# Optimization experiments

Hardware: AMD Instinct MI355X
Metric: run time of the kernel (lower is better)

## Reference

```python
import jax, jax.numpy as jnp
import numpy as np

B, S, D_MODEL, H = 2, 2048, 1024, 16
HD = D_MODEL // H  # head_dim = 64


def setup_inputs() -> dict:
    key = jax.random.key(0)
    kx, kq, kk, kv, ko = jax.random.split(key, 5)
    scale = 1.0 / np.sqrt(D_MODEL)
    return {
        "x": jax.random.normal(kx, (B, S, D_MODEL), dtype=jnp.float32),
        "Wq": jax.random.normal(kq, (D_MODEL, D_MODEL), dtype=jnp.float32) * scale,
        "Wk": jax.random.normal(kk, (D_MODEL, D_MODEL), dtype=jnp.float32) * scale,
        "Wv": jax.random.normal(kv, (D_MODEL, D_MODEL), dtype=jnp.float32) * scale,
        "Wo": jax.random.normal(ko, (D_MODEL, D_MODEL), dtype=jnp.float32) * scale,
        "bo": jnp.zeros((D_MODEL,), dtype=jnp.float32),
    }


def reference(x, Wq, Wk, Wv, Wo, bo):
    b, s, _ = x.shape
    # project and split heads: [b, h, s, hd]
    q = (x @ Wq).reshape(b, s, H, HD).transpose(0, 2, 1, 3)
    k = (x @ Wk).reshape(b, s, H, HD).transpose(0, 2, 1, 3)
    v = (x @ Wv).reshape(b, s, H, HD).transpose(0, 2, 1, 3)
    # full attn score materialization, as in the original module
    scores = jnp.einsum("bhqd,bhkd->bhqk", q, k)
    causal = jnp.triu(jnp.ones((s, s), dtype=bool), k=1)  # True above diagonal -> masked
    scores = jnp.where(causal, -jnp.inf, scores)
    attn = jax.nn.softmax(scores / np.sqrt(HD), axis=-1)  # dropout p=0.0 (eval)
    ctx = jnp.einsum("bhqk,bhkd->bqhd", attn, v).reshape(b, s, D_MODEL)
    return ctx @ Wo + bo
```

## Files before the change

### kernel.cpp

```cpp
#include <hip/hip_runtime.h>
#include <stdint.h>

typedef __bf16 bf16x8 __attribute__((ext_vector_type(8)));
typedef float f32x4 __attribute__((ext_vector_type(4)));

static constexpr int B_ = 2, S_ = 2048, D_ = 1024, H_ = 16, HD_ = 64;
static constexpr int M_ = B_ * S_;
static constexpr size_t HSZ = (size_t)B_ * H_ * S_ * HD_;

#define DEV_INLINE __device__ __forceinline__

#define SC2F (0.125f * 1.4426950408889634f)

DEV_INLINE uint16_t f2bf(float f) {
  __bf16 h = (__bf16)f;
  return __builtin_bit_cast(uint16_t, h);
}

#define GLD16(gptr, lptr)                                                        \
  __builtin_amdgcn_global_load_lds(                                              \
      (const __attribute__((address_space(1))) void*)(gptr),                     \
      (__attribute__((address_space(3))) void*)(lptr), 16, 0, 0)

__global__ void cvt_x_kernel(const float* __restrict__ x, uint16_t* __restrict__ xb) {
  int i = blockIdx.x * 256 + threadIdx.x;
  float4 v = reinterpret_cast<const float4*>(x)[i];
  ushort4 o;
  o.x = f2bf(v.x); o.y = f2bf(v.y); o.z = f2bf(v.z); o.w = f2bf(v.w);
  reinterpret_cast<ushort4*>(xb)[i] = o;
}

__global__ void tr_w_kernel(const float* __restrict__ W0, const float* __restrict__ W1,
                            const float* __restrict__ W2, const float* __restrict__ W3,
                            uint16_t* __restrict__ Wt) {
  __shared__ float tile[32][33];
  const float* W = (blockIdx.z == 0) ? W0 : (blockIdx.z == 1) ? W1
                   : (blockIdx.z == 2) ? W2 : W3;
  uint16_t* dst = Wt + (size_t)blockIdx.z * D_ * D_;
  int c = blockIdx.x * 32 + threadIdx.x;
  int r0 = blockIdx.y * 32;
#pragma unroll
  for (int j = threadIdx.y; j < 32; j += 8)
    tile[j][threadIdx.x] = W[(size_t)(r0 + j) * D_ + c];
  __syncthreads();
  int oc = blockIdx.y * 32 + threadIdx.x;
  int or0 = blockIdx.x * 32;
#pragma unroll
  for (int j = threadIdx.y; j < 32; j += 8)
    dst[(size_t)(or0 + j) * D_ + oc] = f2bf(tile[threadIdx.x][j]);
}

template <int EPI>
__global__ __launch_bounds__(256, 2)
void gemm_bt_kernel(const uint16_t* __restrict__ A, const uint16_t* __restrict__ Bt,
                    uint16_t* __restrict__ Cb, float* __restrict__ Cf,
                    const float* __restrict__ bias, int K) {
  __shared__ uint16_t lds[2][2][128 * 32];
  const int tid = threadIdx.x;
  const int lane = tid & 63;
  const int wid = tid >> 6;
  const int lo = lane & 15, hi = lane >> 4;
  const int row0 = blockIdx.y * 128, col0 = blockIdx.x * 128;
  const int wr = (wid >> 1) * 64, wc = (wid & 1) * 64;

  const uint16_t* gA = A + (size_t)(row0 + (tid >> 2)) * K + (tid & 3) * 8;
  const uint16_t* gB = Bt + (size_t)(col0 + (tid >> 2)) * K + (tid & 3) * 8;

  f32x4 acc[4][4] = {};

  auto stage = [&](int kt, int buf) {
    const uint16_t* a = gA + kt * 32;
    const uint16_t* b = gB + kt * 32;
    char* la = (char*)&lds[buf][0][0] + tid * 16;
    char* lb = (char*)&lds[buf][1][0] + tid * 16;
    GLD16(a, la);
    GLD16(a + (size_t)64 * K, la + 4096);
    GLD16(b, lb);
    GLD16(b + (size_t)64 * K, lb + 4096);
  };

  const int nk = K >> 5;
  stage(0, 0);
  __syncthreads();
  for (int kt = 0; kt < nk; ++kt) {
    const int cur = kt & 1;
    if (kt + 1 < nk) stage(kt + 1, cur ^ 1);
    const uint16_t* lA = &lds[cur][0][0];
    const uint16_t* lB = &lds[cur][1][0];
    bf16x8 af[4], bfr[4];
#pragma unroll
    for (int m = 0; m < 4; ++m)
      af[m] = *(const bf16x8*)(lA + (wr + m * 16 + lo) * 32 + hi * 8);
#pragma unroll
    for (int n = 0; n < 4; ++n)
      bfr[n] = *(const bf16x8*)(lB + (wc + n * 16 + lo) * 32 + hi * 8);
    __builtin_amdgcn_s_setprio(1);
#pragma unroll
    for (int m = 0; m < 4; ++m)
#pragma unroll
      for (int n = 0; n < 4; ++n)
        acc[m][n] = __builtin_amdgcn_mfma_f32_16x16x32_bf16(af[m], bfr[n], acc[m][n], 0, 0, 0);
    __builtin_amdgcn_s_setprio(0);
    __syncthreads();
  }

#pragma unroll
  for (int m = 0; m < 4; ++m)
#pragma unroll
    for (int n = 0; n < 4; ++n) {
      const int gr0 = row0 + wr + m * 16 + hi * 4;
      const int gc = col0 + wc + n * 16 + lo;
      if (EPI == 0) {
        const int which = gc >> 10, c = gc & 1023;
        const int hh = c >> 6, d = c & 63;
        const int bb = gr0 >> 11, s0 = gr0 & 2047;
        if (which == 2) {
          ushort4 pk;
          pk.x = f2bf(acc[m][n][0]); pk.y = f2bf(acc[m][n][1]);
          pk.z = f2bf(acc[m][n][2]); pk.w = f2bf(acc[m][n][3]);
          *reinterpret_cast<ushort4*>(
              &Cb[2 * HSZ + ((size_t)(bb * H_ + hh) * HD_ + d) * S_ + s0]) = pk;
        } else {
          const float qs = (which == 0) ? SC2F : 1.0f;
#pragma unroll
          for (int j = 0; j < 4; ++j)
            Cb[(size_t)which * HSZ + (((size_t)(bb * H_ + hh) * S_ + s0 + j) * HD_ + d)] =
                f2bf(acc[m][n][j] * qs);
        }
      } else {
#pragma unroll
        for (int j = 0; j < 4; ++j)
          Cf[(size_t)(gr0 + j) * D_ + gc] = acc[m][n][j] + bias[gc];
      }
    }
}

__global__ __launch_bounds__(256, 2)
void attn_kernel(const uint16_t* __restrict__ QKV, uint16_t* __restrict__ ctx) {
  __shared__ uint16_t ldsKV[2][2][4096];
  __shared__ uint16_t ldsP[64][72];

  const int tid = threadIdx.x;
  const int lane = tid & 63;
  const int w = tid >> 6;
  const int lo = lane & 15, hi = lane >> 4;

  const int g = blockIdx.x;
  const int p = g & 15, h = (g >> 4) & 15, b = g >> 8;

  const size_t bh = ((size_t)(b * H_ + h)) * S_ * HD_;
  const uint16_t* Q  = QKV + bh;
  const uint16_t* Kp = QKV + HSZ + bh;
  const uint16_t* Vt = QKV + 2 * HSZ + bh;

  auto stage = [&](int kt, int bufi) {
    const uint16_t* gk = Kp + (size_t)(kt * 64 + (tid >> 2)) * HD_ + (tid & 3) * 8;
    char* lk = (char*)&ldsKV[bufi][0][0] + tid * 16;
    GLD16(gk, lk);
    GLD16(gk + 32, lk + 4096);
    const uint16_t* gv = Vt + (size_t)(tid >> 2) * S_ + kt * 64 + (tid & 3) * 8;
    char* lv = (char*)&ldsKV[bufi][1][0] + tid * 16;
    GLD16(gv, lv);
    GLD16(gv + 32, lv + 4096);
  };

  auto sweep = [&](int qt, int nkv) {
    const int q0w = qt * 64 + w * 16;
    bf16x8 qf[2];
#pragma unroll
    for (int ks = 0; ks < 2; ++ks)
      qf[ks] = *(const bf16x8*)(Q + (size_t)(q0w + lo) * HD_ + ks * 32 + hi * 8);

    f32x4 acco[4] = {};
    float mstate = -1e30f, lstate = 0.f;

    stage(0, 0);
    __syncthreads();
    int buf = 0;
    for (int kt = 0; kt < nkv; ++kt) {
      if (kt + 1 < nkv) stage(kt + 1, buf ^ 1);

      const uint16_t* lK = &ldsKV[buf][0][0];
      bf16x8 ak[4][2];
#pragma unroll
      for (int n = 0; n < 4; ++n)
#pragma unroll
        for (int ks = 0; ks < 2; ++ks)
          ak[n][ks] = *(const bf16x8*)(lK + ks * 2048 + (n * 16 + lo) * 32 + hi * 8);

      f32x4 st[4];
      __builtin_amdgcn_s_setprio(1);
#pragma unroll
      for (int n = 0; n < 4; ++n) {
        f32x4 z = {};
        z = __builtin_amdgcn_mfma_f32_16x16x32_bf16(ak[n][0], qf[0], z, 0, 0, 0);
        st[n] = __builtin_amdgcn_mfma_f32_16x16x32_bf16(ak[n][1], qf[1], z, 0, 0, 0);
      }
      __builtin_amdgcn_s_setprio(0);

      if (kt == nkv - 1) {
        const int qg = q0w + lo;
#pragma unroll
        for (int n = 0; n < 4; ++n)
#pragma unroll
          for (int j = 0; j < 4; ++j) {
            int kvg = kt * 64 + n * 16 + hi * 4 + j;
            if (kvg > qg) st[n][j] = -1e30f;
          }
      }

      float vmax = st[0][0];
#pragma unroll
      for (int n = 0; n < 4; ++n)
#pragma unroll
        for (int j = 0; j < 4; ++j) vmax = fmaxf(vmax, st[n][j]);
      vmax = fmaxf(vmax, __shfl_xor(vmax, 16));
      vmax = fmaxf(vmax, __shfl_xor(vmax, 32));

      if (__any(vmax > mstate + 8.f)) {
        float mnew = fmaxf(mstate, vmax);
        float sc = exp2f(mstate - mnew);
        mstate = mnew;
        lstate *= sc;
#pragma unroll
        for (int nd = 0; nd < 4; ++nd)
#pragma unroll
          for (int j = 0; j < 4; ++j) acco[nd][j] *= sc;
      }

      float rsum = 0.f;
#pragma unroll
      for (int n = 0; n < 4; ++n)
#pragma unroll
        for (int j = 0; j < 4; ++j) {
          float pv = exp2f(st[n][j] - mstate);
          st[n][j] = pv;
          rsum += pv;
        }
      rsum += __shfl_xor(rsum, 16);
      rsum += __shfl_xor(rsum, 32);
      lstate += rsum;

#pragma unroll
      for (int n = 0; n < 4; ++n) {
        ushort4 pk;
        pk.x = f2bf(st[n][0]); pk.y = f2bf(st[n][1]);
        pk.z = f2bf(st[n][2]); pk.w = f2bf(st[n][3]);
        *reinterpret_cast<ushort4*>(&ldsP[w * 16 + lo][n * 16 + hi * 4]) = pk;
      }

      const uint16_t* lV = &ldsKV[buf][1][0];
      bf16x8 ap[2], bv[4][2];
#pragma unroll
      for (int ks = 0; ks < 2; ++ks)
        ap[ks] = *(const bf16x8*)(&ldsP[w * 16 + lo][ks * 32 + hi * 8]);
#pragma unroll
      for (int nd = 0; nd < 4; ++nd)
#pragma unroll
        for (int ks = 0; ks < 2; ++ks)
          bv[nd][ks] = *(const bf16x8*)(lV + ks * 2048 + (nd * 16 + lo) * 32 + hi * 8);
      __builtin_amdgcn_s_setprio(1);
#pragma unroll
      for (int nd = 0; nd < 4; ++nd) {
        acco[nd] = __builtin_amdgcn_mfma_f32_16x16x32_bf16(bv[nd][0], ap[0], acco[nd], 0, 0, 0);
        acco[nd] = __builtin_amdgcn_mfma_f32_16x16x32_bf16(bv[nd][1], ap[1], acco[nd], 0, 0, 0);
      }
      __builtin_amdgcn_s_setprio(0);

      __syncthreads();
      buf ^= 1;
    }

    const float inv = 1.f / lstate;
    uint16_t* crow = ctx + (size_t)(b * S_ + q0w + lo) * D_ + h * HD_;
#pragma unroll
    for (int nd = 0; nd < 4; ++nd) {
      ushort4 pk;
      pk.x = f2bf(acco[nd][0] * inv); pk.y = f2bf(acco[nd][1] * inv);
      pk.z = f2bf(acco[nd][2] * inv); pk.w = f2bf(acco[nd][3] * inv);
      *reinterpret_cast<ushort4*>(crow + nd * 16 + hi * 4) = pk;
    }
  };

  sweep(p, p + 1);
  __syncthreads();
  sweep(31 - p, 32 - p);
}

extern "C" void kernel_launch(void* const* d_in, const int* in_sizes, int n_in,
                              void* d_out, int out_size, void* d_ws, size_t ws_size,
                              hipStream_t stream) {
  (void)in_sizes; (void)n_in; (void)out_size; (void)ws_size;
  const float* x  = (const float*)d_in[0];
  const float* Wq = (const float*)d_in[1];
  const float* Wk = (const float*)d_in[2];
  const float* Wv = (const float*)d_in[3];
  const float* Wo = (const float*)d_in[4];
  const float* bo = (const float*)d_in[5];
  float* out = (float*)d_out;

  uint16_t* ws  = (uint16_t*)d_ws;
  uint16_t* xb  = ws;
  uint16_t* Wt  = xb + (size_t)M_ * D_;
  uint16_t* QKV = Wt + (size_t)4 * D_ * D_;
  uint16_t* ctx = QKV + 3 * HSZ;

  cvt_x_kernel<<<(M_ * D_) / 1024, 256, 0, stream>>>(x, xb);
  tr_w_kernel<<<dim3(32, 32, 4), dim3(32, 8), 0, stream>>>(Wq, Wk, Wv, Wo, Wt);
  gemm_bt_kernel<0><<<dim3(3072 / 128, M_ / 128), 256, 0, stream>>>(xb, Wt, QKV, nullptr, nullptr, D_);
  attn_kernel<<<512, 256, 0, stream>>>(QKV, ctx);
  gemm_bt_kernel<1><<<dim3(D_ / 128, M_ / 128), 256, 0, stream>>>(ctx, Wt + (size_t)3 * D_ * D_, nullptr, out, bo, D_);
}
```

Baseline: 126.7 us.

## Triple-buffer KV staging with swizzled LDS and MFMA-based row sums

The attention kernel moves from double to triple buffering of K/V tiles. The next tile is prefetched two steps ahead, and the full __syncthreads is replaced with explicit vmcnt waits and a raw barrier, so global loads overlap more compute. K/V LDS writes and reads use an XOR swizzle to cut bank conflicts. The softmax denominator is now accumulated by an MFMA against a ones vector on the bf16 P tile instead of scalar sums and shuffles. A max3 reduction tree is also added. The cost is more LDS per block, which may limit occupancy, and a row sum computed from bf16-rounded probabilities.

```diff
diff --git a/kernel.cpp b/kernel.cpp
--- a/kernel.cpp
+++ b/kernel.cpp
@@ -16,6 +16,7 @@
   __bf16 h = (__bf16)f;
   return __builtin_bit_cast(uint16_t, h);
 }
+DEV_INLINE float fmax3(float a, float b, float c) { return fmaxf(fmaxf(a, b), c); }
 
 #define GLD16(gptr, lptr)                                                        \
   __builtin_amdgcn_global_load_lds(                                              \
@@ -137,28 +138,35 @@
 
 __global__ __launch_bounds__(256, 2)
 void attn_kernel(const uint16_t* __restrict__ QKV, uint16_t* __restrict__ ctx) {
-  __shared__ uint16_t ldsKV[2][2][4096];
+  __shared__ uint16_t ldsKV[3][2][4096];
   __shared__ uint16_t ldsP[64][72];
 
   const int tid = threadIdx.x;
   const int lane = tid & 63;
   const int w = tid >> 6;
   const int lo = lane & 15, hi = lane >> 4;
+  const int swz = (hi * 8) ^ ((lo & 6) << 2);
 
   const int g = blockIdx.x;
   const int p = g & 15, h = (g >> 4) & 15, b = g >> 8;
 
-  const size_t bh = ((size_t)(b * H_ + h)) * S_ * HD_;
-  const uint16_t* Q  = QKV + bh;
-  const uint16_t* Kp = QKV + HSZ + bh;
-  const uint16_t* Vt = QKV + 2 * HSZ + bh;
-
+  const size_t bhs = ((size_t)(b * H_ + h)) * S_ * HD_;
+  const uint16_t* Q  = QKV + bhs;
+  const uint16_t* Kp = QKV + HSZ + bhs;
+  const uint16_t* Vt = QKV + 2 * HSZ + bhs;
+
+  bf16x8 ones;
+#pragma unroll
+  for (int e = 0; e < 8; ++e) ones[e] = __builtin_bit_cast(__bf16, (uint16_t)0x3F80);
+
+  const int srow = tid >> 2;
+  const int scol = ((tid & 3) ^ ((tid >> 3) & 3)) * 8;
   auto stage = [&](int kt, int bufi) {
-    const uint16_t* gk = Kp + (size_t)(kt * 64 + (tid >> 2)) * HD_ + (tid & 3) * 8;
+    const uint16_t* gk = Kp + (size_t)(kt * 64 + srow) * HD_ + scol;
     char* lk = (char*)&ldsKV[bufi][0][0] + tid * 16;
     GLD16(gk, lk);
     GLD16(gk + 32, lk + 4096);
-    const uint16_t* gv = Vt + (size_t)(tid >> 2) * S_ + kt * 64 + (tid & 3) * 8;
+    const uint16_t* gv = Vt + (size_t)srow * S_ + kt * 64 + scol;
     char* lv = (char*)&ldsKV[bufi][1][0] + tid * 16;
     GLD16(gv, lv);
     GLD16(gv + 32, lv + 4096);
@@ -166,19 +174,26 @@
 
   auto sweep = [&](int qt, int nkv) {
     const int q0w = qt * 64 + w * 16;
+    const int qg = q0w + lo;
     bf16x8 qf[2];
 #pragma unroll
     for (int ks = 0; ks < 2; ++ks)
-      qf[ks] = *(const bf16x8*)(Q + (size_t)(q0w + lo) * HD_ + ks * 32 + hi * 8);
+      qf[ks] = *(const bf16x8*)(Q + (size_t)qg * HD_ + ks * 32 + hi * 8);
 
     f32x4 acco[4] = {};
-    float mstate = -1e30f, lstate = 0.f;
+    f32x4 lacc = {};
+    float mstate = -1e30f;
 
     stage(0, 0);
-    __syncthreads();
-    int buf = 0;
+    if (1 < nkv) stage(1, 1);
+    asm volatile("s_waitcnt vmcnt(4)" ::: "memory");
+    __builtin_amdgcn_s_barrier();
+    __builtin_amdgcn_sched_barrier(0);
+
     for (int kt = 0; kt < nkv; ++kt) {
-      if (kt + 1 < nkv) stage(kt + 1, buf ^ 1);
+      const int buf = kt % 3;
+      const bool staged = (kt + 2 < nkv);
+      if (staged) stage(kt + 2, (kt + 2) % 3);
 
       const uint16_t* lK = &ldsKV[buf][0][0];
       bf16x8 ak[4][2];
@@ -186,7 +201,7 @@
       for (int n = 0; n < 4; ++n)
 #pragma unroll
         for (int ks = 0; ks < 2; ++ks)
-          ak[n][ks] = *(const bf16x8*)(lK + ks * 2048 + (n * 16 + lo) * 32 + hi * 8);
+          ak[n][ks] = *(const bf16x8*)(lK + ks * 2048 + (n * 16 + lo) * 32 + swz);
 
       f32x4 st[4];
       __builtin_amdgcn_s_setprio(1);
@@ -199,7 +214,6 @@
       __builtin_amdgcn_s_setprio(0);
 
       if (kt == nkv - 1) {
-        const int qg = q0w + lo;
 #pragma unroll
         for (int n = 0; n < 4; ++n)
 #pragma unroll
@@ -209,11 +223,14 @@
           }
       }
 
-      float vmax = st[0][0];
-#pragma unroll
-      for (int n = 0; n < 4; ++n)
-#pragma unroll
-        for (int j = 0; j < 4; ++j) vmax = fmaxf(vmax, st[n][j]);
+      float t0 = fmax3(st[0][0], st[0][1], st[0][2]);
+      float t1 = fmax3(t0, st[0][3], st[1][0]);
+      float t2 = fmax3(t1, st[1][1], st[1][2]);
+      float t3 = fmax3(t2, st[1][3], st[2][0]);
+      float t4 = fmax3(t3, st[2][1], st[2][2]);
+      float t5 = fmax3(t4, st[2][3], st[3][0]);
+      float t6 = fmax3(t5, st[3][1], st[3][2]);
+      float vmax = fmaxf(t6, st[3][3]);
       vmax = fmaxf(vmax, __shfl_xor(vmax, 16));
       vmax = fmaxf(vmax, __shfl_xor(vmax, 32));
 
@@ -221,31 +238,20 @@
         float mnew = fmaxf(mstate, vmax);
         float sc = exp2f(mstate - mnew);
         mstate = mnew;
-        lstate *= sc;
+        lacc *= sc;
 #pragma unroll
         for (int nd = 0; nd < 4; ++nd)
 #pragma unroll
           for (int j = 0; j < 4; ++j) acco[nd][j] *= sc;
       }
-
-      float rsum = 0.f;
-#pragma unroll
-      for (int n = 0; n < 4; ++n)
-#pragma unroll
-        for (int j = 0; j < 4; ++j) {
-          float pv = exp2f(st[n][j] - mstate);
-          st[n][j] = pv;
-          rsum += pv;
-        }
-      rsum += __shfl_xor(rsum, 16);
-      rsum += __shfl_xor(rsum, 32);
-      lstate += rsum;
 
 #pragma unroll
       for (int n = 0; n < 4; ++n) {
         ushort4 pk;
-        pk.x = f2bf(st[n][0]); pk.y = f2bf(st[n][1]);
-        pk.z = f2bf(st[n][2]); pk.w = f2bf(st[n][3]);
+        pk.x = f2bf(exp2f(st[n][0] - mstate));
+        pk.y = f2bf(exp2f(st[n][1] - mstate));
+        pk.z = f2bf(exp2f(st[n][2] - mstate));
+        pk.w = f2bf(exp2f(st[n][3] - mstate));
         *reinterpret_cast<ushort4*>(&ldsP[w * 16 + lo][n * 16 + hi * 4]) = pk;
       }
 
@@ -258,8 +264,10 @@
       for (int nd = 0; nd < 4; ++nd)
 #pragma unroll
         for (int ks = 0; ks < 2; ++ks)
-          bv[nd][ks] = *(const bf16x8*)(lV + ks * 2048 + (nd * 16 + lo) * 32 + hi * 8);
+          bv[nd][ks] = *(const bf16x8*)(lV + ks * 2048 + (nd * 16 + lo) * 32 + swz);
       __builtin_amdgcn_s_setprio(1);
+      lacc = __builtin_amdgcn_mfma_f32_16x16x32_bf16(ones, ap[0], lacc, 0, 0, 0);
+      lacc = __builtin_amdgcn_mfma_f32_16x16x32_bf16(ones, ap[1], lacc, 0, 0, 0);
 #pragma unroll
       for (int nd = 0; nd < 4; ++nd) {
         acco[nd] = __builtin_amdgcn_mfma_f32_16x16x32_bf16(bv[nd][0], ap[0], acco[nd], 0, 0, 0);
@@ -267,12 +275,14 @@
       }
       __builtin_amdgcn_s_setprio(0);
 
-      __syncthreads();
-      buf ^= 1;
+      if (staged) asm volatile("s_waitcnt vmcnt(4)" ::: "memory");
+      else        asm volatile("s_waitcnt vmcnt(0)" ::: "memory");
+      __builtin_amdgcn_s_barrier();
+      __builtin_amdgcn_sched_barrier(0);
     }
 
-    const float inv = 1.f / lstate;
-    uint16_t* crow = ctx + (size_t)(b * S_ + q0w + lo) * D_ + h * HD_;
+    const float inv = 1.f / lacc[0];
+    uint16_t* crow = ctx + (size_t)(b * S_ + qg) * D_ + h * HD_;
 #pragma unroll
     for (int nd = 0; nd < 4; ++nd) {
       ushort4 pk;
```

New measurement: 121.5 us. 4.1% less time.
